# Kernel tuning notes

Hardware: AMD Instinct MI355X
Metric: run time of the kernel (lower is better)

Reference implementation:

```python
import jax, jax.numpy as jnp
import numpy as np

N_TOKENS, D_MODEL, D_FF, N_EXPERTS, TOP_K = 4096, 2048, 1408, 8, 2


def setup_inputs() -> dict:
    key = jax.random.key(0)
    ks = jax.random.split(key, 6)
    s = 0.02
    return {
        "x": jax.random.normal(ks[0], (N_TOKENS, D_MODEL), jnp.float32),
        "topK_indices": jax.random.randint(ks[1], (N_TOKENS, TOP_K), 0, N_EXPERTS, jnp.int32),
        "topK_scores": jax.random.uniform(ks[2], (N_TOKENS, TOP_K), jnp.float32),
        "W_gate": jax.random.normal(ks[3], (N_EXPERTS, D_MODEL, D_FF), jnp.float32) * s,
        "W_up": jax.random.normal(ks[4], (N_EXPERTS, D_MODEL, D_FF), jnp.float32) * s,
        "W_down": jax.random.normal(ks[5], (N_EXPERTS, D_FF, D_MODEL), jnp.float32) * s,
    }


def reference(x, topK_indices, topK_scores, W_gate, W_up, W_down):
    # Combine weights: combine[n, e] = sum over k of score[n, k] where idx[n, k] == e.
    # Mathematically identical to the torch sort/split/index_add dispatch-combine
    # (with multiply_gate_scores=True), expressed densely for a clean jax baseline.
    n = x.shape[0]
    rows = jnp.arange(n)[:, None]  # [N, 1]
    combine = jnp.zeros((n, W_gate.shape[0]), x.dtype).at[rows, topK_indices].add(topK_scores)
    # Per-expert SwiGLU MLP (llama-moe LinearGLUExperts, bias-free).
    h = jax.nn.silu(jnp.einsum("nd,edh->enh", x, W_gate)) * jnp.einsum("nd,edh->enh", x, W_up)
    expert_out = jnp.einsum("enh,ehd->end", h, W_down)  # [E, N, D]
    y = jnp.einsum("ne,end->nd", combine, expert_out)  # weighted scatter-add combine
    return y
```

## Files before the change

kernel.cpp:

```cpp
#include <hip/hip_runtime.h>
#include <hip/hip_bf16.h>


#define NTOK 4096
#define DMODEL 2048
#define DFF 1408
#define NEXP 8
#define TOPK 2
#define NSLOT (NTOK * TOPK)
#define MAX_TILES 160
#define NTILE_A 40
#define NTILE_B 72
#define NY1 11
#define NY2 16

typedef short bf16x8 __attribute__((ext_vector_type(8)));
typedef float f32x4 __attribute__((ext_vector_type(4)));

#define MFMA16(a, b, c) __builtin_amdgcn_mfma_f32_16x16x32_bf16(a, b, c, 0, 0, 0)

__device__ inline void async16(const void* g, void* l) {
    __builtin_amdgcn_global_load_lds(
        (const __attribute__((address_space(1))) void*)g,
        (__attribute__((address_space(3))) void*)l, 16, 0, 0);
}

__device__ inline int xcd_swz(int bid, int nblk) {
    int q = nblk >> 3, r = nblk & 7;
    int x = bid & 7, p = bid >> 3;
    return (x < r ? x * (q + 1) : r * (q + 1) + (x - r) * q) + p;
}

__global__ __launch_bounds__(256) void route_kernel(
    const int* __restrict__ idx, const float* __restrict__ scores,
    int* __restrict__ metaA, int* __restrict__ metaB,
    int* __restrict__ slot_token, float* __restrict__ slot_score,
    int bmA, int bmB)
{
    __shared__ int counts[NEXP];
    __shared__ int cursor[NEXP];
    int t = threadIdx.x;
    if (t < NEXP) counts[t] = 0;
    __syncthreads();
    for (int i = t; i < NSLOT; i += 256) atomicAdd(&counts[idx[i]], 1);
    __syncthreads();
    if (t == 0) {
        int off = 0, nt = 0;
        for (int e = 0; e < NEXP; e++) {
            cursor[e] = off;
            int c = counts[e];
            for (int s = 0; s < c && nt < MAX_TILES; s += bmA) {
                metaA[1 + nt * 3 + 0] = e;
                metaA[1 + nt * 3 + 1] = off + s;
                metaA[1 + nt * 3 + 2] = min(bmA, c - s);
                nt++;
            }
            off += c;
        }
        metaA[0] = nt;
        off = 0; nt = 0;
        for (int e = 0; e < NEXP; e++) {
            int c = counts[e];
            for (int s = 0; s < c && nt < MAX_TILES; s += bmB) {
                metaB[1 + nt * 3 + 0] = e;
                metaB[1 + nt * 3 + 1] = off + s;
                metaB[1 + nt * 3 + 2] = min(bmB, c - s);
                nt++;
            }
            off += c;
        }
        metaB[0] = nt;
    }
    __syncthreads();
    for (int i = t; i < NSLOT; i += 256) {
        int e = idx[i];
        int pos = atomicAdd(&cursor[e], 1);
        slot_token[pos] = i / TOPK;
        slot_score[pos] = scores[i];
    }
}

__global__ __launch_bounds__(256) void convert_x(
    const float* __restrict__ x, __hip_bfloat16* __restrict__ xb)
{
    int i = blockIdx.x * 256 + threadIdx.x;
    float4 v = reinterpret_cast<const float4*>(x)[i];
    __hip_bfloat16 o[4] = {(__hip_bfloat16)v.x, (__hip_bfloat16)v.y,
                           (__hip_bfloat16)v.z, (__hip_bfloat16)v.w};
    *reinterpret_cast<uint2*>(&xb[(size_t)i * 4]) = *reinterpret_cast<uint2*>(o);
}

__global__ __launch_bounds__(256) void transpose_convert(
    const float* __restrict__ in, __hip_bfloat16* __restrict__ out, int R, int C)
{
    __shared__ __hip_bfloat16 t[64][72];
    const size_t base = (size_t)blockIdx.z * R * C;
    const int c0 = blockIdx.x * 64, r0 = blockIdx.y * 64;
    const int tid = threadIdx.x;
    const int rl = tid >> 4, c4 = (tid & 15) * 4;
    #pragma unroll
    for (int j = 0; j < 4; j++) {
        int r = rl + j * 16;
        float4 v = *reinterpret_cast<const float4*>(&in[base + (size_t)(r0 + r) * C + c0 + c4]);
        t[c4 + 0][r] = (__hip_bfloat16)v.x;
        t[c4 + 1][r] = (__hip_bfloat16)v.y;
        t[c4 + 2][r] = (__hip_bfloat16)v.z;
        t[c4 + 3][r] = (__hip_bfloat16)v.w;
    }
    __syncthreads();
    const int nl = tid >> 3, k8 = (tid & 7) * 8;
    #pragma unroll
    for (int j = 0; j < 2; j++) {
        int n = nl + j * 32;
        const uint* p = reinterpret_cast<const uint*>(&t[n][k8]);
        uint4 o = {p[0], p[1], p[2], p[3]};
        *reinterpret_cast<uint4*>(&out[base + (size_t)(c0 + n) * R + r0 + k8]) = o;
    }
}

__global__ __launch_bounds__(512, 2) void moe_gemm1_fast(
    const __hip_bfloat16* __restrict__ xb,
    const __hip_bfloat16* __restrict__ WgT, const __hip_bfloat16* __restrict__ WuT,
    const int* __restrict__ meta, const int* __restrict__ slot_token,
    __hip_bfloat16* __restrict__ h)
{
    const int swz = xcd_swz(blockIdx.x, NTILE_A * NY1);
    const int tile = swz / NY1, yb = swz % NY1;
    if (tile >= meta[0]) return;
    const int e = meta[1 + tile * 3], slot0 = meta[2 + tile * 3], rows = meta[3 + tile * 3];
    const int n0 = yb * 128;

    __shared__ __hip_bfloat16 As[2][256][64];
    __shared__ __hip_bfloat16 Bgs[2][128][64];
    __shared__ __hip_bfloat16 Bus[2][128][64];

    const int tid = threadIdx.x, lane = tid & 63, w = tid >> 6;
    const int wm = w >> 2, wn = w & 3, l15 = lane & 15, lg = lane >> 4;
    const int swb = l15 & 7;

    uint aoff[4], boff[2];
    #pragma unroll
    for (int i = 0; i < 4; i++) {
        int chunk = tid + i * 512;
        int r = chunk >> 3;
        int rc = r < rows ? r : rows - 1;
        int slot8 = (chunk & 7) ^ (r & 7);
        aoff[i] = (uint)(slot_token[slot0 + rc] * (DMODEL * 2) + slot8 * 16);
    }
    #pragma unroll
    for (int i = 0; i < 2; i++) {
        int chunk = tid + i * 512;
        int n = chunk >> 3;
        int slot8 = (chunk & 7) ^ (n & 7);
        boff[i] = (uint)((n0 + n) * (DMODEL * 2) + slot8 * 16);
    }
    const char* xbp = (const char*)xb;
    const char* wgp = (const char*)(WgT + (size_t)e * DFF * DMODEL);
    const char* wup = (const char*)(WuT + (size_t)e * DFF * DMODEL);

    f32x4 ag[8][2] = {};
    f32x4 au[8][2] = {};

    auto stage = [&](int kt, int buf) {
        const int kb = kt * 128;
        char* ab = (char*)As[buf]  + w * 1024;
        char* gb = (char*)Bgs[buf] + w * 1024;
        char* ub = (char*)Bus[buf] + w * 1024;
        #pragma unroll
        for (int i = 0; i < 4; i++) async16(xbp + aoff[i] + kb, ab + i * 8192);
        #pragma unroll
        for (int i = 0; i < 2; i++) {
            async16(wgp + boff[i] + kb, gb + i * 8192);
            async16(wup + boff[i] + kb, ub + i * 8192);
        }
    };

    constexpr int NT = DMODEL / 64;
    stage(0, 0);
    stage(1, 1);

    for (int kt = 0; kt < NT; ++kt) {
        const int cur = kt & 1;
        if (kt < NT - 1) asm volatile("s_waitcnt vmcnt(8)" ::: "memory");
        else             asm volatile("s_waitcnt vmcnt(0)" ::: "memory");
        __builtin_amdgcn_s_barrier();

        const int cb0 = (lg ^ swb) * 16;
        const int cb1 = ((4 + lg) ^ swb) * 16;
        bf16x8 a0[8], bg0[2], bu0[2], a1[8], bg1[2], bu1[2];
        #pragma unroll
        for (int mf = 0; mf < 8; mf++)
            a0[mf] = *(const bf16x8*)((const char*)&As[cur][wm * 128 + mf * 16 + l15][0] + cb0);
        #pragma unroll
        for (int nf = 0; nf < 2; nf++) {
            bg0[nf] = *(const bf16x8*)((const char*)&Bgs[cur][wn * 32 + nf * 16 + l15][0] + cb0);
            bu0[nf] = *(const bf16x8*)((const char*)&Bus[cur][wn * 32 + nf * 16 + l15][0] + cb0);
        }
        __builtin_amdgcn_sched_barrier(0);
        #pragma unroll
        for (int mf = 0; mf < 8; mf++)
            a1[mf] = *(const bf16x8*)((const char*)&As[cur][wm * 128 + mf * 16 + l15][0] + cb1);
        #pragma unroll
        for (int nf = 0; nf < 2; nf++) {
            bg1[nf] = *(const bf16x8*)((const char*)&Bgs[cur][wn * 32 + nf * 16 + l15][0] + cb1);
            bu1[nf] = *(const bf16x8*)((const char*)&Bus[cur][wn * 32 + nf * 16 + l15][0] + cb1);
        }
        asm volatile("s_waitcnt lgkmcnt(12)" ::: "memory");
        __builtin_amdgcn_sched_barrier(0);
        __builtin_amdgcn_s_setprio(1);
        #pragma unroll
        for (int mf = 0; mf < 8; mf++)
            #pragma unroll
            for (int nf = 0; nf < 2; nf++) {
                ag[mf][nf] = MFMA16(a0[mf], bg0[nf], ag[mf][nf]);
                au[mf][nf] = MFMA16(a0[mf], bu0[nf], au[mf][nf]);
            }
        __builtin_amdgcn_s_setprio(0);
        asm volatile("s_waitcnt lgkmcnt(0)" ::: "memory");
        __builtin_amdgcn_sched_barrier(0);
        __builtin_amdgcn_s_barrier();
        if (kt + 2 < NT) stage(kt + 2, cur);
        __builtin_amdgcn_s_setprio(1);
        #pragma unroll
        for (int mf = 0; mf < 8; mf++)
            #pragma unroll
            for (int nf = 0; nf < 2; nf++) {
                ag[mf][nf] = MFMA16(a1[mf], bg1[nf], ag[mf][nf]);
                au[mf][nf] = MFMA16(a1[mf], bu1[nf], au[mf][nf]);
            }
        __builtin_amdgcn_s_setprio(0);
    }

    #pragma unroll
    for (int mf = 0; mf < 8; mf++) {
        #pragma unroll
        for (int j = 0; j < 4; j++) {
            int r = wm * 128 + mf * 16 + lg * 4 + j;
            if (r < rows) {
                size_t hrow = (size_t)(slot0 + r) * DFF + n0 + wn * 32;
                #pragma unroll
                for (int nf = 0; nf < 2; nf++) {
                    float g = ag[mf][nf][j], u = au[mf][nf][j];
                    float hv = g / (1.0f + __expf(-g)) * u;
                    h[hrow + nf * 16 + l15] = (__hip_bfloat16)hv;
                }
            }
        }
    }
}

__global__ __launch_bounds__(256, 2) void moe_gemm2_fast(
    const __hip_bfloat16* __restrict__ h, const __hip_bfloat16* __restrict__ WdT,
    const int* __restrict__ meta, const int* __restrict__ slot_token,
    const float* __restrict__ slot_score, float* __restrict__ out)
{
    const int swz = xcd_swz(blockIdx.x, NTILE_B * NY2);
    const int tile = swz / NY2, yb = swz % NY2;
    if (tile >= meta[0]) return;
    const int e = meta[1 + tile * 3], slot0 = meta[2 + tile * 3], rows = meta[3 + tile * 3];
    const int n0 = yb * 128;

    __shared__ __hip_bfloat16 Ah[2][128][64];
    __shared__ __hip_bfloat16 Bd[2][128][64];

    const int tid = threadIdx.x, lane = tid & 63, w = tid >> 6;
    const int wm = w >> 1, wn = w & 1, l15 = lane & 15, lg = lane >> 4;
    const int swb = l15 & 7;

    uint aoff[4], boff[4];
    #pragma unroll
    for (int i = 0; i < 4; i++) {
        int chunk = tid + i * 256;
        int r = chunk >> 3;
        int rc = r < rows ? r : rows - 1;
        int slot8 = (chunk & 7) ^ (r & 7);
        aoff[i] = (uint)((slot0 + rc) * (DFF * 2) + slot8 * 16);
        boff[i] = (uint)((n0 + r) * (DFF * 2) + slot8 * 16);
    }
    const char* hp  = (const char*)h;
    const char* wdp = (const char*)(WdT + (size_t)e * DMODEL * DFF);

    f32x4 acc[4][4] = {};

    auto stage = [&](int kt, int buf) {
        const int kb = kt * 128;
        char* ab = (char*)Ah[buf] + w * 1024;
        char* bb = (char*)Bd[buf] + w * 1024;
        #pragma unroll
        for (int i = 0; i < 4; i++) {
            async16(hp  + aoff[i] + kb, ab + i * 4096);
            async16(wdp + boff[i] + kb, bb + i * 4096);
        }
    };

    constexpr int NT = DFF / 64;
    stage(0, 0);
    stage(1, 1);

    for (int kt = 0; kt < NT; ++kt) {
        const int cur = kt & 1;
        if (kt < NT - 1) asm volatile("s_waitcnt vmcnt(8)" ::: "memory");
        else             asm volatile("s_waitcnt vmcnt(0)" ::: "memory");
        __builtin_amdgcn_s_barrier();

        const int cb0 = (lg ^ swb) * 16;
        const int cb1 = ((4 + lg) ^ swb) * 16;
        bf16x8 a0[4], b0[4], a1[4], b1[4];
        #pragma unroll
        for (int mf = 0; mf < 4; mf++) {
            a0[mf] = *(const bf16x8*)((const char*)&Ah[cur][wm * 64 + mf * 16 + l15][0] + cb0);
            b0[mf] = *(const bf16x8*)((const char*)&Bd[cur][wn * 64 + mf * 16 + l15][0] + cb0);
        }
        __builtin_amdgcn_sched_barrier(0);
        #pragma unroll
        for (int mf = 0; mf < 4; mf++) {
            a1[mf] = *(const bf16x8*)((const char*)&Ah[cur][wm * 64 + mf * 16 + l15][0] + cb1);
            b1[mf] = *(const bf16x8*)((const char*)&Bd[cur][wn * 64 + mf * 16 + l15][0] + cb1);
        }
        asm volatile("s_waitcnt lgkmcnt(8)" ::: "memory");
        __builtin_amdgcn_sched_barrier(0);
        __builtin_amdgcn_s_setprio(1);
        #pragma unroll
        for (int mf = 0; mf < 4; mf++)
            #pragma unroll
            for (int nf = 0; nf < 4; nf++)
                acc[mf][nf] = MFMA16(a0[mf], b0[nf], acc[mf][nf]);
        __builtin_amdgcn_s_setprio(0);
        asm volatile("s_waitcnt lgkmcnt(0)" ::: "memory");
        __builtin_amdgcn_sched_barrier(0);
        __builtin_amdgcn_s_barrier();
        if (kt + 2 < NT) stage(kt + 2, cur);
        __builtin_amdgcn_s_setprio(1);
        #pragma unroll
        for (int mf = 0; mf < 4; mf++)
            #pragma unroll
            for (int nf = 0; nf < 4; nf++)
                acc[mf][nf] = MFMA16(a1[mf], b1[nf], acc[mf][nf]);
        __builtin_amdgcn_s_setprio(0);
    }

    #pragma unroll
    for (int mf = 0; mf < 4; mf++) {
        #pragma unroll
        for (int j = 0; j < 4; j++) {
            int r = wm * 64 + mf * 16 + lg * 4 + j;
            if (r < rows) {
                int slot = slot0 + r;
                int tok = slot_token[slot];
                float s = slot_score[slot];
                float* orow = out + (size_t)tok * DMODEL + n0 + wn * 64;
                #pragma unroll
                for (int nf = 0; nf < 4; nf++)
                    atomicAdd(&orow[nf * 16 + l15], s * acc[mf][nf][j]);
            }
        }
    }
}

__global__ __launch_bounds__(256) void moe_gemm1(
    const float* __restrict__ x, const float* __restrict__ Wg, const float* __restrict__ Wu,
    const int* __restrict__ meta, const int* __restrict__ slot_token,
    __hip_bfloat16* __restrict__ h)
{
    int tile = blockIdx.x;
    if (tile >= meta[0]) return;
    const int e = meta[1 + tile * 3], slot0 = meta[2 + tile * 3], rows = meta[3 + tile * 3];
    const int n0 = blockIdx.y * 64;
    __shared__ __hip_bfloat16 As[64][72];
    __shared__ __hip_bfloat16 Bgs[64][72];
    __shared__ __hip_bfloat16 Bus[64][72];
    const int tid = threadIdx.x, lane = tid & 63, w = tid >> 6;
    const int wm = w >> 1, wn = w & 1, l15 = lane & 15, lg = lane >> 4;
    const float* __restrict__ WgE = Wg + (size_t)e * DMODEL * DFF;
    const float* __restrict__ WuE = Wu + (size_t)e * DMODEL * DFF;
    f32x4 acc_g[2][2] = {};
    f32x4 acc_u[2][2] = {};
    for (int k0 = 0; k0 < DMODEL; k0 += 64) {
        __syncthreads();
        #pragma unroll
        for (int j = 0; j < 4; j++) {
            int linear = tid + j * 256;
            int r = linear >> 4, c4 = (linear & 15) * 4;
            int tok = (r < rows) ? slot_token[slot0 + r] : 0;
            float4 v = *reinterpret_cast<const float4*>(&x[(size_t)tok * DMODEL + k0 + c4]);
            As[r][c4 + 0] = (__hip_bfloat16)v.x; As[r][c4 + 1] = (__hip_bfloat16)v.y;
            As[r][c4 + 2] = (__hip_bfloat16)v.z; As[r][c4 + 3] = (__hip_bfloat16)v.w;
        }
        #pragma unroll
        for (int j = 0; j < 4; j++) {
            int linear = tid + j * 256;
            int k = linear >> 4, n4 = (linear & 15) * 4;
            float4 vg = *reinterpret_cast<const float4*>(&WgE[(size_t)(k0 + k) * DFF + n0 + n4]);
            Bgs[n4 + 0][k] = (__hip_bfloat16)vg.x; Bgs[n4 + 1][k] = (__hip_bfloat16)vg.y;
            Bgs[n4 + 2][k] = (__hip_bfloat16)vg.z; Bgs[n4 + 3][k] = (__hip_bfloat16)vg.w;
            float4 vu = *reinterpret_cast<const float4*>(&WuE[(size_t)(k0 + k) * DFF + n0 + n4]);
            Bus[n4 + 0][k] = (__hip_bfloat16)vu.x; Bus[n4 + 1][k] = (__hip_bfloat16)vu.y;
            Bus[n4 + 2][k] = (__hip_bfloat16)vu.z; Bus[n4 + 3][k] = (__hip_bfloat16)vu.w;
        }
        __syncthreads();
        #pragma unroll
        for (int kk = 0; kk < 2; kk++) {
            bf16x8 a[2], bg[2], bu[2];
            #pragma unroll
            for (int mf = 0; mf < 2; mf++)
                a[mf] = *reinterpret_cast<const bf16x8*>(&As[wm * 32 + mf * 16 + l15][kk * 32 + lg * 8]);
            #pragma unroll
            for (int nf = 0; nf < 2; nf++) {
                bg[nf] = *reinterpret_cast<const bf16x8*>(&Bgs[wn * 32 + nf * 16 + l15][kk * 32 + lg * 8]);
                bu[nf] = *reinterpret_cast<const bf16x8*>(&Bus[wn * 32 + nf * 16 + l15][kk * 32 + lg * 8]);
            }
            #pragma unroll
            for (int mf = 0; mf < 2; mf++)
                #pragma unroll
                for (int nf = 0; nf < 2; nf++) {
                    acc_g[mf][nf] = MFMA16(a[mf], bg[nf], acc_g[mf][nf]);
                    acc_u[mf][nf] = MFMA16(a[mf], bu[nf], acc_u[mf][nf]);
                }
        }
    }
    #pragma unroll
    for (int mf = 0; mf < 2; mf++)
        #pragma unroll
        for (int nf = 0; nf < 2; nf++)
            #pragma unroll
            for (int j = 0; j < 4; j++) {
                int r = wm * 32 + mf * 16 + lg * 4 + j;
                int c = wn * 32 + nf * 16 + l15;
                if (r < rows) {
                    float g = acc_g[mf][nf][j], u = acc_u[mf][nf][j];
                    h[(size_t)(slot0 + r) * DFF + n0 + c] = (__hip_bfloat16)(g / (1.0f + __expf(-g)) * u);
                }
            }
}

__global__ __launch_bounds__(256) void moe_gemm2(
    const __hip_bfloat16* __restrict__ h, const float* __restrict__ Wd,
    const int* __restrict__ meta, const int* __restrict__ slot_token,
    const float* __restrict__ slot_score, float* __restrict__ out)
{
    int tile = blockIdx.x;
    if (tile >= meta[0]) return;
    const int e = meta[1 + tile * 3], slot0 = meta[2 + tile * 3], rows = meta[3 + tile * 3];
    const int n0 = blockIdx.y * 64;
    __shared__ __hip_bfloat16 As[64][72];
    __shared__ __hip_bfloat16 Bs[64][72];
    const int tid = threadIdx.x, lane = tid & 63, w = tid >> 6;
    const int wm = w >> 1, wn = w & 1, l15 = lane & 15, lg = lane >> 4;
    const float* __restrict__ WdE = Wd + (size_t)e * DFF * DMODEL;
    f32x4 acc[2][2] = {};
    for (int k0 = 0; k0 < DFF; k0 += 64) {
        __syncthreads();
        #pragma unroll
        for (int j = 0; j < 2; j++) {
            int linear = tid + j * 256;
            int r = linear >> 3, c8 = (linear & 7) * 8;
            bf16x8 v = *reinterpret_cast<const bf16x8*>(&h[(size_t)(slot0 + r) * DFF + k0 + c8]);
            *reinterpret_cast<bf16x8*>(&As[r][c8]) = v;
        }
        #pragma unroll
        for (int j = 0; j < 4; j++) {
            int linear = tid + j * 256;
            int k = linear >> 4, n4 = (linear & 15) * 4;
            float4 v = *reinterpret_cast<const float4*>(&WdE[(size_t)(k0 + k) * DMODEL + n0 + n4]);
            Bs[n4 + 0][k] = (__hip_bfloat16)v.x; Bs[n4 + 1][k] = (__hip_bfloat16)v.y;
            Bs[n4 + 2][k] = (__hip_bfloat16)v.z; Bs[n4 + 3][k] = (__hip_bfloat16)v.w;
        }
        __syncthreads();
        #pragma unroll
        for (int kk = 0; kk < 2; kk++) {
            bf16x8 a[2], b[2];
            #pragma unroll
            for (int mf = 0; mf < 2; mf++)
                a[mf] = *reinterpret_cast<const bf16x8*>(&As[wm * 32 + mf * 16 + l15][kk * 32 + lg * 8]);
            #pragma unroll
            for (int nf = 0; nf < 2; nf++)
                b[nf] = *reinterpret_cast<const bf16x8*>(&Bs[wn * 32 + nf * 16 + l15][kk * 32 + lg * 8]);
            #pragma unroll
            for (int mf = 0; mf < 2; mf++)
                #pragma unroll
                for (int nf = 0; nf < 2; nf++)
                    acc[mf][nf] = MFMA16(a[mf], b[nf], acc[mf][nf]);
        }
    }
    #pragma unroll
    for (int mf = 0; mf < 2; mf++)
        #pragma unroll
        for (int nf = 0; nf < 2; nf++)
            #pragma unroll
            for (int j = 0; j < 4; j++) {
                int r = wm * 32 + mf * 16 + lg * 4 + j;
                int c = wn * 32 + nf * 16 + l15;
                if (r < rows) {
                    int slot = slot0 + r;
                    atomicAdd(&out[(size_t)slot_token[slot] * DMODEL + n0 + c],
                              acc[mf][nf][j] * slot_score[slot]);
                }
            }
}

extern "C" void kernel_launch(void* const* d_in, const int* in_sizes, int n_in,
                              void* d_out, int out_size, void* d_ws, size_t ws_size,
                              hipStream_t stream) {
    const float* x      = (const float*)d_in[0];
    const int*   idx    = (const int*)d_in[1];
    const float* scores = (const float*)d_in[2];
    const float* Wg     = (const float*)d_in[3];
    const float* Wu     = (const float*)d_in[4];
    const float* Wd     = (const float*)d_in[5];
    float* out = (float*)d_out;

    char* ws = (char*)d_ws;
    int*   metaA      = (int*)ws;
    int*   metaB      = (int*)(ws + 4096);
    int*   slot_token = (int*)(ws + 8192);
    float* slot_score = (float*)(ws + 8192 + 32768);

    const size_t XB_OFF = (size_t)1 << 20;
    const size_t HB_OFF = (size_t)20 << 20;
    const size_t WG_OFF = (size_t)44 << 20;
    const size_t WU_OFF = (size_t)92 << 20;
    const size_t WD_OFF = (size_t)140 << 20;
    const size_t NEED   = (size_t)187 << 20;
    const bool fast = ws_size >= NEED;

    hipMemsetAsync(d_out, 0, (size_t)NTOK * DMODEL * sizeof(float), stream);
    route_kernel<<<1, 256, 0, stream>>>(idx, scores, metaA, metaB, slot_token, slot_score,
                                        fast ? 256 : 64, fast ? 128 : 64);

    if (fast) {
        __hip_bfloat16* xb  = (__hip_bfloat16*)(ws + XB_OFF);
        __hip_bfloat16* hb  = (__hip_bfloat16*)(ws + HB_OFF);
        __hip_bfloat16* WgT = (__hip_bfloat16*)(ws + WG_OFF);
        __hip_bfloat16* WuT = (__hip_bfloat16*)(ws + WU_OFF);
        __hip_bfloat16* WdT = (__hip_bfloat16*)(ws + WD_OFF);

        dim3 td(DMODEL / 64, DFF / 64, NEXP);
        transpose_convert<<<td, 256, 0, stream>>>(Wd, WdT, DFF, DMODEL);
        dim3 tg(DFF / 64, DMODEL / 64, NEXP);
        transpose_convert<<<tg, 256, 0, stream>>>(Wg, WgT, DMODEL, DFF);
        transpose_convert<<<tg, 256, 0, stream>>>(Wu, WuT, DMODEL, DFF);
        convert_x<<<(NTOK * DMODEL / 4) / 256, 256, 0, stream>>>(x, xb);

        moe_gemm1_fast<<<NTILE_A * NY1, 512, 0, stream>>>(xb, WgT, WuT, metaA, slot_token, hb);
        moe_gemm2_fast<<<NTILE_B * NY2, 256, 0, stream>>>(hb, WdT, metaB, slot_token, slot_score, out);
    } else {
        __hip_bfloat16* hb = (__hip_bfloat16*)(ws + HB_OFF);
        dim3 g1(NSLOT / 64 + NEXP, DFF / 64);
        moe_gemm1<<<g1, 256, 0, stream>>>(x, Wg, Wu, metaA, slot_token, hb);
        dim3 g2(NSLOT / 64 + NEXP, DMODEL / 64);
        moe_gemm2<<<g2, 256, 0, stream>>>(hb, Wd, metaB, slot_token, slot_score, out);
    }
}
```

Measured before the change: 361.4 us.

## Replace atomic scatter-add with bf16 slot output and per-token combine kernel

The down-projection GEMM now writes unweighted per-slot results as bf16 into a scratch buffer that reuses the gate-weight workspace. A new combine kernel then uses the token-to-slot map from routing to take the weighted sum of each token's two slot rows, which removes the output memset and the fp32 atomics. Both GEMM inner loops also switch from a two-phase prefetch of LDS fragments to smaller sub-steps that wait for LDS and sync with a barrier each step. This adds a kernel launch and extra traffic, rounds expert outputs to bf16 before combining, and the extra barriers may reduce overlap.

```diff
diff --git a/kernel.cpp b/kernel.cpp
--- a/kernel.cpp
+++ b/kernel.cpp
@@ -35,7 +35,7 @@
     const int* __restrict__ idx, const float* __restrict__ scores,
     int* __restrict__ metaA, int* __restrict__ metaB,
     int* __restrict__ slot_token, float* __restrict__ slot_score,
-    int bmA, int bmB)
+    int* __restrict__ tok_slot, int bmA, int bmB)
 {
     __shared__ int counts[NEXP];
     __shared__ int cursor[NEXP];
@@ -77,6 +77,7 @@
         int pos = atomicAdd(&cursor[e], 1);
         slot_token[pos] = i / TOPK;
         slot_score[pos] = scores[i];
+        tok_slot[i] = pos;
     }
 }
 
@@ -118,6 +119,28 @@
     }
 }
 
+__global__ __launch_bounds__(256) void combine_kernel(
+    const __hip_bfloat16* __restrict__ so, const int* __restrict__ tok_slot,
+    const float* __restrict__ slot_score, float* __restrict__ out)
+{
+    const int tok = blockIdx.x;
+    const int c = threadIdx.x * 8;
+    const int s0 = tok_slot[tok * 2 + 0], s1 = tok_slot[tok * 2 + 1];
+    const float w0 = slot_score[s0], w1 = slot_score[s1];
+    bf16x8 v0 = *reinterpret_cast<const bf16x8*>(&so[(size_t)s0 * DMODEL + c]);
+    bf16x8 v1 = *reinterpret_cast<const bf16x8*>(&so[(size_t)s1 * DMODEL + c]);
+    float res[8];
+    #pragma unroll
+    for (int j = 0; j < 8; j++) {
+        float f0 = __uint_as_float(((uint)(unsigned short)v0[j]) << 16);
+        float f1 = __uint_as_float(((uint)(unsigned short)v1[j]) << 16);
+        res[j] = w0 * f0 + w1 * f1;
+    }
+    float4* dst = reinterpret_cast<float4*>(&out[(size_t)tok * DMODEL + c]);
+    dst[0] = *reinterpret_cast<float4*>(&res[0]);
+    dst[1] = *reinterpret_cast<float4*>(&res[4]);
+}
+
 __global__ __launch_bounds__(512, 2) void moe_gemm1_fast(
     const __hip_bfloat16* __restrict__ xb,
     const __hip_bfloat16* __restrict__ WgT, const __hip_bfloat16* __restrict__ WuT,
@@ -185,50 +208,38 @@
         else             asm volatile("s_waitcnt vmcnt(0)" ::: "memory");
         __builtin_amdgcn_s_barrier();
 
-        const int cb0 = (lg ^ swb) * 16;
-        const int cb1 = ((4 + lg) ^ swb) * 16;
-        bf16x8 a0[8], bg0[2], bu0[2], a1[8], bg1[2], bu1[2];
-        #pragma unroll
-        for (int mf = 0; mf < 8; mf++)
-            a0[mf] = *(const bf16x8*)((const char*)&As[cur][wm * 128 + mf * 16 + l15][0] + cb0);
-        #pragma unroll
-        for (int nf = 0; nf < 2; nf++) {
-            bg0[nf] = *(const bf16x8*)((const char*)&Bgs[cur][wn * 32 + nf * 16 + l15][0] + cb0);
-            bu0[nf] = *(const bf16x8*)((const char*)&Bus[cur][wn * 32 + nf * 16 + l15][0] + cb0);
-        }
-        __builtin_amdgcn_sched_barrier(0);
-        #pragma unroll
-        for (int mf = 0; mf < 8; mf++)
-            a1[mf] = *(const bf16x8*)((const char*)&As[cur][wm * 128 + mf * 16 + l15][0] + cb1);
-        #pragma unroll
-        for (int nf = 0; nf < 2; nf++) {
-            bg1[nf] = *(const bf16x8*)((const char*)&Bgs[cur][wn * 32 + nf * 16 + l15][0] + cb1);
-            bu1[nf] = *(const bf16x8*)((const char*)&Bus[cur][wn * 32 + nf * 16 + l15][0] + cb1);
-        }
-        asm volatile("s_waitcnt lgkmcnt(12)" ::: "memory");
-        __builtin_amdgcn_sched_barrier(0);
-        __builtin_amdgcn_s_setprio(1);
-        #pragma unroll
-        for (int mf = 0; mf < 8; mf++)
-            #pragma unroll
-            for (int nf = 0; nf < 2; nf++) {
-                ag[mf][nf] = MFMA16(a0[mf], bg0[nf], ag[mf][nf]);
-                au[mf][nf] = MFMA16(a0[mf], bu0[nf], au[mf][nf]);
-            }
-        __builtin_amdgcn_s_setprio(0);
-        asm volatile("s_waitcnt lgkmcnt(0)" ::: "memory");
-        __builtin_amdgcn_sched_barrier(0);
-        __builtin_amdgcn_s_barrier();
+        bf16x8 bgk[2], buk[2];
+        #pragma unroll
+        for (int p = 0; p < 4; p++) {
+            const int kk = p >> 1, mh = p & 1;
+            const int cb = ((kk * 4 + lg) ^ swb) * 16;
+            bf16x8 a[4];
+            #pragma unroll
+            for (int mi = 0; mi < 4; mi++)
+                a[mi] = *(const bf16x8*)((const char*)&As[cur][wm * 128 + (mh * 4 + mi) * 16 + l15][0] + cb);
+            if (mh == 0) {
+                #pragma unroll
+                for (int nf = 0; nf < 2; nf++) {
+                    bgk[nf] = *(const bf16x8*)((const char*)&Bgs[cur][wn * 32 + nf * 16 + l15][0] + cb);
+                    buk[nf] = *(const bf16x8*)((const char*)&Bus[cur][wn * 32 + nf * 16 + l15][0] + cb);
+                }
+            }
+            asm volatile("s_waitcnt lgkmcnt(0)" ::: "memory");
+            __builtin_amdgcn_sched_barrier(0);
+            __builtin_amdgcn_s_setprio(1);
+            #pragma unroll
+            for (int mi = 0; mi < 4; mi++) {
+                const int mf = mh * 4 + mi;
+                #pragma unroll
+                for (int nf = 0; nf < 2; nf++) {
+                    ag[mf][nf] = MFMA16(a[mi], bgk[nf], ag[mf][nf]);
+                    au[mf][nf] = MFMA16(a[mi], buk[nf], au[mf][nf]);
+                }
+            }
+            __builtin_amdgcn_s_setprio(0);
+            __builtin_amdgcn_s_barrier();
+        }
         if (kt + 2 < NT) stage(kt + 2, cur);
-        __builtin_amdgcn_s_setprio(1);
-        #pragma unroll
-        for (int mf = 0; mf < 8; mf++)
-            #pragma unroll
-            for (int nf = 0; nf < 2; nf++) {
-                ag[mf][nf] = MFMA16(a1[mf], bg1[nf], ag[mf][nf]);
-                au[mf][nf] = MFMA16(a1[mf], bu1[nf], au[mf][nf]);
-            }
-        __builtin_amdgcn_s_setprio(0);
     }
 
     #pragma unroll
@@ -251,8 +262,7 @@
 
 __global__ __launch_bounds__(256, 2) void moe_gemm2_fast(
     const __hip_bfloat16* __restrict__ h, const __hip_bfloat16* __restrict__ WdT,
-    const int* __restrict__ meta, const int* __restrict__ slot_token,
-    const float* __restrict__ slot_score, float* __restrict__ out)
+    const int* __restrict__ meta, __hip_bfloat16* __restrict__ so)
 {
     const int swz = xcd_swz(blockIdx.x, NTILE_B * NY2);
     const int tile = swz / NY2, yb = swz % NY2;
@@ -303,40 +313,27 @@
         else             asm volatile("s_waitcnt vmcnt(0)" ::: "memory");
         __builtin_amdgcn_s_barrier();
 
-        const int cb0 = (lg ^ swb) * 16;
-        const int cb1 = ((4 + lg) ^ swb) * 16;
-        bf16x8 a0[4], b0[4], a1[4], b1[4];
-        #pragma unroll
-        for (int mf = 0; mf < 4; mf++) {
-            a0[mf] = *(const bf16x8*)((const char*)&Ah[cur][wm * 64 + mf * 16 + l15][0] + cb0);
-            b0[mf] = *(const bf16x8*)((const char*)&Bd[cur][wn * 64 + mf * 16 + l15][0] + cb0);
-        }
-        __builtin_amdgcn_sched_barrier(0);
-        #pragma unroll
-        for (int mf = 0; mf < 4; mf++) {
-            a1[mf] = *(const bf16x8*)((const char*)&Ah[cur][wm * 64 + mf * 16 + l15][0] + cb1);
-            b1[mf] = *(const bf16x8*)((const char*)&Bd[cur][wn * 64 + mf * 16 + l15][0] + cb1);
-        }
-        asm volatile("s_waitcnt lgkmcnt(8)" ::: "memory");
-        __builtin_amdgcn_sched_barrier(0);
-        __builtin_amdgcn_s_setprio(1);
-        #pragma unroll
-        for (int mf = 0; mf < 4; mf++)
-            #pragma unroll
-            for (int nf = 0; nf < 4; nf++)
-                acc[mf][nf] = MFMA16(a0[mf], b0[nf], acc[mf][nf]);
-        __builtin_amdgcn_s_setprio(0);
-        asm volatile("s_waitcnt lgkmcnt(0)" ::: "memory");
-        __builtin_amdgcn_sched_barrier(0);
-        __builtin_amdgcn_s_barrier();
+        #pragma unroll
+        for (int p = 0; p < 2; p++) {
+            const int cb = ((p * 4 + lg) ^ swb) * 16;
+            bf16x8 a[4], b[4];
+            #pragma unroll
+            for (int mf = 0; mf < 4; mf++) {
+                a[mf] = *(const bf16x8*)((const char*)&Ah[cur][wm * 64 + mf * 16 + l15][0] + cb);
+                b[mf] = *(const bf16x8*)((const char*)&Bd[cur][wn * 64 + mf * 16 + l15][0] + cb);
+            }
+            asm volatile("s_waitcnt lgkmcnt(0)" ::: "memory");
+            __builtin_amdgcn_sched_barrier(0);
+            __builtin_amdgcn_s_setprio(1);
+            #pragma unroll
+            for (int mf = 0; mf < 4; mf++)
+                #pragma unroll
+                for (int nf = 0; nf < 4; nf++)
+                    acc[mf][nf] = MFMA16(a[mf], b[nf], acc[mf][nf]);
+            __builtin_amdgcn_s_setprio(0);
+            __builtin_amdgcn_s_barrier();
+        }
         if (kt + 2 < NT) stage(kt + 2, cur);
-        __builtin_amdgcn_s_setprio(1);
-        #pragma unroll
-        for (int mf = 0; mf < 4; mf++)
-            #pragma unroll
-            for (int nf = 0; nf < 4; nf++)
-                acc[mf][nf] = MFMA16(a1[mf], b1[nf], acc[mf][nf]);
-        __builtin_amdgcn_s_setprio(0);
     }
 
     #pragma unroll
@@ -345,13 +342,10 @@
         for (int j = 0; j < 4; j++) {
             int r = wm * 64 + mf * 16 + lg * 4 + j;
             if (r < rows) {
-                int slot = slot0 + r;
-                int tok = slot_token[slot];
-                float s = slot_score[slot];
-                float* orow = out + (size_t)tok * DMODEL + n0 + wn * 64;
+                size_t orow = (size_t)(slot0 + r) * DMODEL + n0 + wn * 64;
                 #pragma unroll
                 for (int nf = 0; nf < 4; nf++)
-                    atomicAdd(&orow[nf * 16 + l15], s * acc[mf][nf][j]);
+                    so[orow + nf * 16 + l15] = (__hip_bfloat16)acc[mf][nf][j];
             }
         }
     }
@@ -513,7 +507,8 @@
     int*   metaA      = (int*)ws;
     int*   metaB      = (int*)(ws + 4096);
     int*   slot_token = (int*)(ws + 8192);
-    float* slot_score = (float*)(ws + 8192 + 32768);
+    float* slot_score = (float*)(ws + 8192 + 40960);
+    int*   tok_slot   = (int*)(ws + 8192 + 81920);
 
     const size_t XB_OFF = (size_t)1 << 20;
     const size_t HB_OFF = (size_t)20 << 20;
@@ -523,9 +518,8 @@
     const size_t NEED   = (size_t)187 << 20;
     const bool fast = ws_size >= NEED;
 
-    hipMemsetAsync(d_out, 0, (size_t)NTOK * DMODEL * sizeof(float), stream);
     route_kernel<<<1, 256, 0, stream>>>(idx, scores, metaA, metaB, slot_token, slot_score,
-                                        fast ? 256 : 64, fast ? 128 : 64);
+                                        tok_slot, fast ? 256 : 64, fast ? 128 : 64);
 
     if (fast) {
         __hip_bfloat16* xb  = (__hip_bfloat16*)(ws + XB_OFF);
@@ -533,6 +527,7 @@
         __hip_bfloat16* WgT = (__hip_bfloat16*)(ws + WG_OFF);
         __hip_bfloat16* WuT = (__hip_bfloat16*)(ws + WU_OFF);
         __hip_bfloat16* WdT = (__hip_bfloat16*)(ws + WD_OFF);
+        __hip_bfloat16* sot = (__hip_bfloat16*)(ws + WG_OFF);
 
         dim3 td(DMODEL / 64, DFF / 64, NEXP);
         transpose_convert<<<td, 256, 0, stream>>>(Wd, WdT, DFF, DMODEL);
@@ -542,9 +537,11 @@
         convert_x<<<(NTOK * DMODEL / 4) / 256, 256, 0, stream>>>(x, xb);
 
         moe_gemm1_fast<<<NTILE_A * NY1, 512, 0, stream>>>(xb, WgT, WuT, metaA, slot_token, hb);
-        moe_gemm2_fast<<<NTILE_B * NY2, 256, 0, stream>>>(hb, WdT, metaB, slot_token, slot_score, out);
+        moe_gemm2_fast<<<NTILE_B * NY2, 256, 0, stream>>>(hb, WdT, metaB, sot);
+        combine_kernel<<<NTOK, 256, 0, stream>>>(sot, tok_slot, slot_score, out);
     } else {
         __hip_bfloat16* hb = (__hip_bfloat16*)(ws + HB_OFF);
+        hipMemsetAsync(d_out, 0, (size_t)NTOK * DMODEL * sizeof(float), stream);
         dim3 g1(NSLOT / 64 + NEXP, DFF / 64);
         moe_gemm1<<<g1, 256, 0, stream>>>(x, Wg, Wu, metaA, slot_token, hb);
         dim3 g2(NSLOT / 64 + NEXP, DMODEL / 64);
```

New measurement: 364.6 us. About the same (+0.9%).
